# Kernel optimization log

Measured on AMD Instinct MI355X. Metric: run time of the kernel, lower is better.

Reference implementation:

```python
import jax, jax.numpy as jnp
import numpy as np

DIM = 256
QK = 256
HEADS = 8
NWIN = 16
TOPK = 4
MLP_RATIO = 4
SCALE = QK ** -0.5


def setup_inputs() -> dict:
    key = jax.random.key(0)
    ks = jax.random.split(key, 8)
    p = lambda k, shp: jax.random.normal(k, shp, jnp.float32) * 0.02
    hid = MLP_RATIO * DIM
    return {
        "x": jax.random.normal(ks[0], (8, DIM, 64, 64), jnp.float32),
        # to_q / to_kv : 1x1 Conv2d_BN (eval-mode BN with running stats 0/1 -> scale+shift)
        "wq": p(ks[1], (QK, DIM)), "gq": jnp.ones((QK,), jnp.float32), "bq": jnp.zeros((QK,), jnp.float32),
        "wkv": p(ks[2], (QK + DIM, DIM)), "gkv": jnp.ones((QK + DIM,), jnp.float32), "bkv": jnp.zeros((QK + DIM,), jnp.float32),
        # LEPE depthwise 5x5 conv
        "w_lepe": p(ks[3], (DIM, 1, 5, 5)), "b_lepe": jnp.zeros((DIM,), jnp.float32),
        # Mlp: fc1(1x1 Conv2d_BN) -> dwconv3x3 -> ReLU -> fc2(1x1 Conv2d_BN)
        "w_fc1": p(ks[4], (hid, DIM)), "g_fc1": jnp.ones((hid,), jnp.float32), "b_fc1": jnp.zeros((hid,), jnp.float32),
        "w_dw": p(ks[5], (hid, 1, 3, 3)), "b_dw": jnp.zeros((hid,), jnp.float32),
        "w_fc2": p(ks[6], (DIM, hid)), "g_fc2": jnp.ones((DIM,), jnp.float32), "b_fc2": jnp.zeros((DIM,), jnp.float32),
    }


def _dwconv(x, w, b, pad):
    # x: NCHW, w: (C,1,k,k) depthwise
    out = jax.lax.conv_general_dilated(
        x, w, (1, 1), [(pad, pad), (pad, pad)],
        feature_group_count=x.shape[1],
        dimension_numbers=("NCHW", "OIHW", "NCHW"))
    return out + b[None, :, None, None]


def _bra(x, wq, gq, bq, wkv, gkv, bkv, w_lepe, b_lepe):
    # Bi-Level Routing Attention. x: NCHW
    N, C, H, W = x.shape
    j = i = NWIN
    h, w_ = H // j, W // i          # per-window spatial (4,4)
    p2, w2 = j * i, h * w_          # 256 windows, 16 tokens/window
    xh = x.transpose(0, 2, 3, 1)    # NHWC
    # windowize: (N, p2, h, w, C)
    xw = xh.reshape(N, j, h, i, w_, C).transpose(0, 1, 3, 2, 4, 5).reshape(N, p2, h, w_, C)
    # 1x1 conv + BN(eval: stats 0/1) == matmul * gamma + beta
    q = (xw @ wq.T) * gq + bq                    # (N,p2,h,w,QK)
    kv = (xw @ wkv.T) * gkv + bkv                # (N,p2,h,w,QK+C)
    q_pix = q.reshape(N, p2, w2, QK)
    kv_pix = kv.reshape(N, p2, w2, QK + C)       # identity kv_down
    q_win = q.mean((2, 3))                       # (N,p2,QK)
    k_win = kv[..., :QK].mean((2, 3))            # (N,p2,QK)
    # LEPE on V in full-image layout
    v_img = kv[..., QK:].reshape(N, j, i, h, w_, C).transpose(0, 1, 3, 2, 4, 5).reshape(N, H, W, C)
    lepe = _dwconv(v_img.transpose(0, 3, 1, 2), w_lepe, b_lepe, 2).transpose(0, 2, 3, 1)  # NHWC
    # window-level topk routing (detached, non-differentiable)
    qd = jax.lax.stop_gradient(q_win)
    kd = jax.lax.stop_gradient(k_win)
    logit = (qd * SCALE) @ kd.transpose(0, 2, 1)            # (N,p2,p2)
    _, r_idx = jax.lax.top_k(logit, TOPK)                   # (N,p2,TOPK); r_weight unused (mul_weight='none')
    # gather selected KV windows: (N,p2,TOPK,w2,QK+C)
    kv_sel = jax.vmap(lambda kvp, idx: kvp[idx])(kv_pix, r_idx)
    ch_k, ch_v = QK // HEADS, C // HEADS
    k_sel = kv_sel[..., :QK].reshape(N, p2, TOPK * w2, HEADS, ch_k).transpose(0, 1, 3, 2, 4)
    v_sel = kv_sel[..., QK:].reshape(N, p2, TOPK * w2, HEADS, ch_v).transpose(0, 1, 3, 2, 4)
    qh = q_pix.reshape(N, p2, w2, HEADS, ch_k).transpose(0, 1, 3, 2, 4)
    attn = jax.nn.softmax(jnp.einsum("npmqc,npmkc->npmqk", qh * SCALE, k_sel), axis=-1)
    out = jnp.einsum("npmqk,npmkc->npmqc", attn, v_sel)     # (N,p2,HEADS,w2,ch_v)
    out = out.transpose(0, 1, 3, 2, 4).reshape(N, j, i, h, w_, C)
    out = out.transpose(0, 1, 3, 2, 4, 5).reshape(N, H, W, C)
    out = out + lepe                                         # wo = Identity
    return out.transpose(0, 3, 1, 2)                         # NCHW


def reference(x, wq, gq, bq, wkv, gkv, bkv, w_lepe, b_lepe,
              w_fc1, g_fc1, b_fc1, w_dw, b_dw, w_fc2, g_fc2, b_fc2):
    # top_Block: x = x + attn(x); x = x + mlp(x)   (drop_path inactive in eval)
    x = x + _bra(x, wq, gq, bq, wkv, gkv, bkv, w_lepe, b_lepe)
    h1 = jnp.einsum("nchw,dc->ndhw", x, w_fc1) * g_fc1[None, :, None, None] + b_fc1[None, :, None, None]
    h1 = jax.nn.relu(_dwconv(h1, w_dw, b_dw, 1))
    h2 = jnp.einsum("nchw,dc->ndhw", h1, w_fc2) * g_fc2[None, :, None, None] + b_fc2[None, :, None, None]
    return x + h2
```

## Files before the change

kernel.cpp:

```cpp
#include <hip/hip_runtime.h>
#include <hip/hip_bf16.h>

#define NBATCH 8
#define CDIM 256
#define HH 64
#define WW 64
#define HWSZ 4096
#define TT 32768
#define QKVD 768
#define TOPK 4
#define HID 1024
#define ATTN_SCALE 0.0625f

typedef __hip_bfloat16 bf16;
typedef __attribute__((ext_vector_type(8))) short s8v;
typedef __attribute__((ext_vector_type(4))) float f4v;

__device__ __forceinline__ float toF(bf16 v) { return __bfloat162float(v); }
__device__ __forceinline__ bf16  toB(float v) { return __float2bfloat16(v); }

__global__ void k_prep(const float* __restrict__ wq, const float* __restrict__ gq,
                       const float* __restrict__ wkv, const float* __restrict__ gkv,
                       const float* __restrict__ wfc1, const float* __restrict__ gfc1,
                       const float* __restrict__ wfc2, const float* __restrict__ gfc2,
                       const float* __restrict__ bq, const float* __restrict__ bkv,
                       const float* __restrict__ w_dw, const float* __restrict__ b_dw,
                       bf16* __restrict__ wbqkv, bf16* __restrict__ wbfc1,
                       bf16* __restrict__ wbfc2, float* __restrict__ bias768,
                       float* __restrict__ wdwT) {
    int i = blockIdx.x * 256 + threadIdx.x;
    if (i < 196608) {
        int r = i >> 8;
        float g = (r < 256) ? gq[r] : gkv[r - 256];
        float w = (r < 256) ? wq[i] : wkv[i - 65536];
        wbqkv[i] = toB(w * g);
        if (i < 768) bias768[i] = (i < 256) ? bq[i] : bkv[i - 256];
    } else if (i < 458752) {
        int j = i - 196608;
        wbfc1[j] = toB(wfc1[j] * gfc1[j >> 8]);
    } else if (i < 720896) {
        int j = i - 458752;
        wbfc2[j] = toB(wfc2[j] * gfc2[j >> 10]);
    } else if (i < 731136) {
        int j = i - 720896;
        int cg = j / 80, r = j - cg * 80;
        wdwT[j] = (r < 72) ? w_dw[(cg * 8 + r / 9) * 9 + (r % 9)]
                           : b_dw[cg * 8 + (r - 72)];
    }
}

__global__ void k_xt(const float* __restrict__ x, bf16* __restrict__ xt) {
    __shared__ float tile[32][33];
    int s0 = blockIdx.x * 32, c0 = blockIdx.y * 32, n = blockIdx.z;
    int tx = threadIdx.x, ty = threadIdx.y;
#pragma unroll
    for (int r = 0; r < 4; r++)
        tile[ty + r * 8][tx] = x[(size_t)n * CDIM * HWSZ + (size_t)(c0 + ty + r * 8) * HWSZ + s0 + tx];
    __syncthreads();
#pragma unroll
    for (int r = 0; r < 4; r++)
        xt[((size_t)n * HWSZ + s0 + ty + r * 8) * CDIM + c0 + tx] = toB(tile[tx][ty + r * 8]);
}

__global__ void k_xwin(const float* __restrict__ x, float* __restrict__ xwin) {
    int b = blockIdx.x;
    int n = b >> 8, c = b & 255;
    int p = threadIdx.x, wy = p >> 4, wx = p & 15;
    const float* pl = x + ((size_t)n * CDIM + c) * HWSZ;
    float s = 0.f;
#pragma unroll
    for (int dy = 0; dy < 4; dy++)
#pragma unroll
        for (int dx = 0; dx < 4; dx++)
            s += pl[(wy * 4 + dy) * WW + wx * 4 + dx];
    xwin[((size_t)(n << 8) + p) * 256 + c] = s * 0.0625f;
}

__global__ void k_qkwin(const float* __restrict__ xwin,
                        const float* __restrict__ wq, const float* __restrict__ wkv,
                        const float* __restrict__ gq, const float* __restrict__ bq,
                        const float* __restrict__ gkv, const float* __restrict__ bkv,
                        float* __restrict__ qkwin) {
    __shared__ float As[16][68];
    __shared__ float Bs[16][68];
    int m0 = blockIdx.x * 64, n0 = blockIdx.y * 64;
    int tid = threadIdx.x;
    int tx = tid & 15, ty = tid >> 4;
    float acc[4][4] = {};
    for (int k0 = 0; k0 < 256; k0 += 16) {
#pragma unroll
        for (int r = 0; r < 4; r++) {
            int lin = tid + r * 256;
            int row = lin >> 4, kk = lin & 15;
            As[kk][row] = xwin[(size_t)(m0 + row) * 256 + k0 + kk];
            int n = n0 + row;
            const float* wr = (n < 256) ? (wq + (size_t)n * 256) : (wkv + (size_t)(n - 256) * 256);
            Bs[kk][row] = wr[k0 + kk];
        }
        __syncthreads();
#pragma unroll
        for (int kk = 0; kk < 16; kk++) {
            float a[4], bb[4];
#pragma unroll
            for (int i = 0; i < 4; i++) a[i] = As[kk][tx * 4 + i];
#pragma unroll
            for (int j = 0; j < 4; j++) bb[j] = Bs[kk][ty * 4 + j];
#pragma unroll
            for (int i = 0; i < 4; i++)
#pragma unroll
                for (int j = 0; j < 4; j++) acc[i][j] += a[i] * bb[j];
        }
        __syncthreads();
    }
#pragma unroll
    for (int j = 0; j < 4; j++) {
        int n = n0 + ty * 4 + j;
        float gg = (n < 256) ? gq[n] : gkv[n - 256];
        float bb = (n < 256) ? bq[n] : bkv[n - 256];
#pragma unroll
        for (int i = 0; i < 4; i++)
            qkwin[(size_t)(m0 + tx * 4 + i) * 512 + n] = acc[i][j] * gg + bb;
    }
}

__global__ void k_logits(const float* __restrict__ qkwin, float* __restrict__ logits) {
    __shared__ float As[16][68];
    __shared__ float Bs[16][68];
    int m0 = blockIdx.x * 64, n0 = blockIdx.y * 64, img = blockIdx.z;
    const float* base = qkwin + (size_t)(img << 8) * 512;
    int tid = threadIdx.x;
    int tx = tid & 15, ty = tid >> 4;
    float acc[4][4] = {};
    for (int k0 = 0; k0 < 256; k0 += 16) {
#pragma unroll
        for (int r = 0; r < 4; r++) {
            int lin = tid + r * 256;
            int row = lin >> 4, kk = lin & 15;
            As[kk][row] = base[(size_t)(m0 + row) * 512 + k0 + kk];
            Bs[kk][row] = base[(size_t)(n0 + row) * 512 + 256 + k0 + kk];
        }
        __syncthreads();
#pragma unroll
        for (int kk = 0; kk < 16; kk++) {
            float a[4], bb[4];
#pragma unroll
            for (int i = 0; i < 4; i++) a[i] = As[kk][tx * 4 + i];
#pragma unroll
            for (int j = 0; j < 4; j++) bb[j] = Bs[kk][ty * 4 + j];
#pragma unroll
            for (int i = 0; i < 4; i++)
#pragma unroll
                for (int j = 0; j < 4; j++) acc[i][j] += a[i] * bb[j];
        }
        __syncthreads();
    }
    float* Lr = logits + (size_t)(img << 8) * 256;
#pragma unroll
    for (int j = 0; j < 4; j++)
#pragma unroll
        for (int i = 0; i < 4; i++)
            Lr[(size_t)(m0 + tx * 4 + i) * 256 + n0 + ty * 4 + j] = acc[i][j];
}

__global__ __launch_bounds__(256) void k_topk(const float* __restrict__ logits,
                                              int* __restrict__ topk) {
    int row = blockIdx.x * 4 + (threadIdx.x >> 6);
    int lane = threadIdx.x & 63;
    float4 v4 = *(const float4*)(logits + (size_t)row * 256 + lane * 4);
    float v[4] = {v4.x, v4.y, v4.z, v4.w};
#pragma unroll
    for (int sel = 0; sel < TOPK; sel++) {
        float mv = v[0]; int mi = lane * 4;
#pragma unroll
        for (int j = 1; j < 4; j++)
            if (v[j] > mv) { mv = v[j]; mi = lane * 4 + j; }
#pragma unroll
        for (int off = 1; off < 64; off <<= 1) {
            float ov = __shfl_xor(mv, off);
            int oi = __shfl_xor(mi, off);
            if (ov > mv || (ov == mv && oi < mi)) { mv = ov; mi = oi; }
        }
        if (lane == 0) topk[(size_t)row * TOPK + sel] = mi;
        if ((mi >> 2) == lane) v[mi & 3] = -INFINITY;
    }
}

template <int BM, int BN, int OUTMODE>
__global__ __launch_bounds__(256) void k_mfma(const bf16* __restrict__ A,
                                              const bf16* __restrict__ Wb,
                                              const float* __restrict__ bias,
                                              bf16* __restrict__ out,
                                              bf16* __restrict__ out2,
                                              int M, int N, int K) {
    constexpr int WROWS = BM / 2, WCOLS = BN / 2;
    constexpr int WM = WROWS / 16, WN = WCOLS / 16;
    constexpr int CA = (BM * 4) / 256;
    constexpr int CB = (BN * 4) / 256;
    __shared__ bf16 As[BM * 32];
    __shared__ bf16 Bs[BN * 32];
    int gx = gridDim.x;
    int lin = blockIdx.x + blockIdx.y * gx;
    int tot = gx * gridDim.y;
    int cpx = tot >> 3;
    int swz = (lin & 7) * cpx + (lin >> 3);
    int m0 = (swz % gx) * BM, n0 = (swz / gx) * BN;
    int tid = threadIdx.x;
    int w = tid >> 6, lane = tid & 63;
    int wr = w >> 1, wc = w & 1;
    int lm = lane & 15, lq = lane >> 4;
    f4v acc[WM][WN];
#pragma unroll
    for (int i = 0; i < WM; i++)
#pragma unroll
        for (int j = 0; j < WN; j++) acc[i][j] = (f4v){0.f, 0.f, 0.f, 0.f};

    for (int k0 = 0; k0 < K; k0 += 32) {
        s8v va[CA], vb[CB];
#pragma unroll
        for (int q = 0; q < CA; q++) {
            int c = tid + q * 256, row = c >> 2, col = c & 3;
            va[q] = *(const s8v*)(A + (size_t)(m0 + row) * K + k0 + col * 8);
        }
#pragma unroll
        for (int q = 0; q < CB; q++) {
            int c = tid + q * 256, row = c >> 2, col = c & 3;
            vb[q] = *(const s8v*)(Wb + (size_t)(n0 + row) * K + k0 + col * 8);
        }
        __syncthreads();
#pragma unroll
        for (int q = 0; q < CA; q++) {
            int c = tid + q * 256, row = c >> 2, col = c & 3;
            *(s8v*)&As[row * 32 + col * 8] = va[q];
        }
#pragma unroll
        for (int q = 0; q < CB; q++) {
            int c = tid + q * 256, row = c >> 2, col = c & 3;
            *(s8v*)&Bs[row * 32 + col * 8] = vb[q];
        }
        __syncthreads();
        s8v af[WM], bfr[WN];
#pragma unroll
        for (int i = 0; i < WM; i++)
            af[i] = *(const s8v*)&As[(wr * WROWS + i * 16 + lm) * 32 + lq * 8];
#pragma unroll
        for (int j = 0; j < WN; j++)
            bfr[j] = *(const s8v*)&Bs[(wc * WCOLS + j * 16 + lm) * 32 + lq * 8];
#pragma unroll
        for (int i = 0; i < WM; i++)
#pragma unroll
            for (int j = 0; j < WN; j++)
                acc[i][j] = __builtin_amdgcn_mfma_f32_16x16x32_bf16(af[i], bfr[j], acc[i][j], 0, 0, 0);
    }
#pragma unroll
    for (int j = 0; j < WN; j++) {
        int n = n0 + wc * WCOLS + j * 16 + lm;
        float bb = bias[n];
#pragma unroll
        for (int i = 0; i < WM; i++) {
            int mb = m0 + wr * WROWS + i * 16 + lq * 4;
#pragma unroll
            for (int r = 0; r < 4; r++)
                out[(size_t)(mb + r) * N + n] = toB(acc[i][j][r] + bb);
            if (OUTMODE == 1 && n >= 512) {
                bf16* dst = out2 + ((size_t)(mb >> 12) * CDIM + (n - 512)) * HWSZ + (mb & 4095);
#pragma unroll
                for (int r = 0; r < 4; r++) dst[r] = toB(acc[i][j][r] + bb);
            }
        }
    }
}

__global__ void k_lepe_pl(bf16* __restrict__ vpl, const float* __restrict__ w_lepe,
                          const float* __restrict__ b_lepe) {
    __shared__ float pl[HWSZ];
    int b = blockIdx.x;
    int n = b >> 8, c = b & 255;
    int tid = threadIdx.x;
    bf16* plane = vpl + ((size_t)n * CDIM + c) * HWSZ;
    const uint4* p4 = (const uint4*)plane;
#pragma unroll
    for (int k = 0; k < 2; k++) {
        uint4 v = p4[tid + k * 256];
        const bf16* pv = (const bf16*)&v;
        int base = (tid + k * 256) * 8;
#pragma unroll
        for (int e = 0; e < 8; e++) pl[base + e] = toF(pv[e]);
    }
    float wreg[25];
#pragma unroll
    for (int i = 0; i < 25; i++) wreg[i] = w_lepe[c * 25 + i];
    float bias = b_lepe[c];
    __syncthreads();
#pragma unroll
    for (int k = 0; k < 2; k++) {
        int s = (tid + k * 256) * 8;
        int y = s >> 6, x0 = s & 63;
        uint4 pk;
        bf16* pb = (bf16*)&pk;
#pragma unroll
        for (int e = 0; e < 8; e++) {
            int xb = x0 + e;
            float acc = bias;
#pragma unroll
            for (int dy = -2; dy <= 2; dy++) {
                int yy = y + dy;
                if (yy < 0 || yy >= HH) continue;
#pragma unroll
                for (int dx = -2; dx <= 2; dx++) {
                    int xx = xb + dx;
                    if (xx < 0 || xx >= WW) continue;
                    acc += pl[yy * 64 + xx] * wreg[(dy + 2) * 5 + (dx + 2)];
                }
            }
            pb[e] = toB(acc);
        }
        ((uint4*)plane)[tid + k * 256] = pk;
    }
}

__global__ __launch_bounds__(256) void k_attn(const bf16* __restrict__ qkv,
                                              const int* __restrict__ topk,
                                              bf16* __restrict__ attnout) {
    __shared__ bf16 vst[256][72];
    __shared__ bf16 plds[4][16][72];
    __shared__ float lsm[4][16];
    __shared__ int toks[64];
    int b = blockIdx.x;
    int n = b >> 8, p = b & 255;
    int wy = p >> 4, wx = p & 15;
    int tid = threadIdx.x;
    if (tid < 64) {
        int rp = topk[((size_t)(n << 8) + p) * TOPK + (tid >> 4)] & 255;
        int st = tid & 15;
        toks[tid] = ((rp >> 4) * 4 + (st >> 2)) * WW + (rp & 15) * 4 + (st & 3);
    }
    __syncthreads();
    const bf16* qbase = qkv + (size_t)n * HWSZ * QKVD;
    {
        int kt = tid & 63, jj = tid >> 6;
#pragma unroll
        for (int pass = 0; pass < 8; pass++) {
            int d0 = pass * 32 + jj * 8;
            uint4 v = *(const uint4*)(qbase + (size_t)toks[kt] * QKVD + 512 + d0);
            const bf16* pv = (const bf16*)&v;
#pragma unroll
            for (int e = 0; e < 8; e++) vst[d0 + e][kt] = pv[e];
        }
    }
    __syncthreads();
    int w = tid >> 6, lane = tid & 63;
    int ln = lane & 15, lq = lane >> 4;
    int myS = (wy * 4 + (ln >> 2)) * WW + wx * 4 + (ln & 3);
    const f4v fz = {0.f, 0.f, 0.f, 0.f};
    for (int hh = 0; hh < 2; hh++) {
        int h = w * 2 + hh;
        s8v qf = *(const s8v*)(qbase + (size_t)myS * QKVD + h * 32 + lq * 8);
        f4v st4[4];
#pragma unroll
        for (int t = 0; t < 4; t++) {
            s8v kf = *(const s8v*)(qbase + (size_t)toks[t * 16 + ln] * QKVD + 256 + h * 32 + lq * 8);
            st4[t] = __builtin_amdgcn_mfma_f32_16x16x32_bf16(kf, qf, fz, 0, 0, 0);
        }
        float mx = -INFINITY;
#pragma unroll
        for (int t = 0; t < 4; t++)
#pragma unroll
            for (int r = 0; r < 4; r++) mx = fmaxf(mx, st4[t][r]);
        mx = fmaxf(mx, __shfl_xor(mx, 16));
        mx = fmaxf(mx, __shfl_xor(mx, 32));
        mx *= ATTN_SCALE;
        float sum = 0.f;
#pragma unroll
        for (int t = 0; t < 4; t++)
#pragma unroll
            for (int r = 0; r < 4; r++) {
                float pp = __expf(st4[t][r] * ATTN_SCALE - mx);
                sum += pp;
                plds[w][ln][t * 16 + lq * 4 + r] = toB(pp);
            }
        sum += __shfl_xor(sum, 16);
        sum += __shfl_xor(sum, 32);
        if (lq == 0) lsm[w][ln] = sum;
        __syncthreads();
        s8v ap0 = *(const s8v*)&plds[w][ln][lq * 8];
        s8v ap1 = *(const s8v*)&plds[w][ln][32 + lq * 8];
#pragma unroll
        for (int dt = 0; dt < 2; dt++) {
            int dim = h * 32 + dt * 16 + ln;
            s8v vv0 = *(const s8v*)&vst[dim][lq * 8];
            s8v vv1 = *(const s8v*)&vst[dim][32 + lq * 8];
            f4v o = __builtin_amdgcn_mfma_f32_16x16x32_bf16(ap0, vv0, fz, 0, 0, 0);
            o = __builtin_amdgcn_mfma_f32_16x16x32_bf16(ap1, vv1, o, 0, 0, 0);
#pragma unroll
            for (int r = 0; r < 4; r++) {
                int t = lq * 4 + r;
                float linv = 1.f / lsm[w][t];
                int s = (wy * 4 + (t >> 2)) * WW + wx * 4 + (t & 3);
                attnout[((size_t)n * HWSZ + s) * CDIM + dim] = toB(o[r] * linv);
            }
        }
        __syncthreads();
    }
}

__global__ void k_x1(const bf16* __restrict__ xt, const bf16* __restrict__ lepe,
                     const bf16* __restrict__ attnout, bf16* __restrict__ x1) {
    __shared__ float tile[32][33];
    int s0 = blockIdx.x * 32, c0 = blockIdx.y * 32, n = blockIdx.z;
    int tx = threadIdx.x, ty = threadIdx.y;
#pragma unroll
    for (int r = 0; r < 4; r++) {
        int c = c0 + ty + r * 8;
        tile[ty + r * 8][tx] = toF(lepe[((size_t)n * CDIM + c) * HWSZ + s0 + tx]);
    }
    __syncthreads();
#pragma unroll
    for (int r = 0; r < 4; r++) {
        int s = s0 + ty + r * 8;
        size_t idx = ((size_t)n * HWSZ + s) * CDIM + c0 + tx;
        x1[idx] = toB(toF(xt[idx]) + toF(attnout[idx]) + tile[tx][ty + r * 8]);
    }
}

__global__ __launch_bounds__(256) void k_dw3_t(const bf16* __restrict__ h1,
                                               const float* __restrict__ wdwT,
                                               bf16* __restrict__ h1p) {
    int tid = threadIdx.x;
    int cg = tid & 127;
    int slot = tid >> 7;
    int seg = blockIdx.x;
    int img = blockIdx.y;
    int y = seg >> 2;
    int x0 = ((seg & 3) << 4) + (slot << 3);
    const float* wp = wdwT + cg * 80;
    float w[72], bias[8];
#pragma unroll
    for (int i = 0; i < 72; i++) w[i] = wp[i];
#pragma unroll
    for (int c = 0; c < 8; c++) bias[c] = wp[72 + c];
    const uint4* src = (const uint4*)h1 + (size_t)img * HWSZ * 128;
    uint4* dst = (uint4*)h1p + (size_t)img * HWSZ * 128;
#pragma unroll
    for (int xi = 0; xi < 8; xi++) {
        int x = x0 + xi;
        float o[8];
#pragma unroll
        for (int c = 0; c < 8; c++) o[c] = bias[c];
#pragma unroll
        for (int dy = -1; dy <= 1; dy++) {
            int yy = y + dy;
            if (yy < 0 || yy >= HH) continue;
#pragma unroll
            for (int dx = -1; dx <= 1; dx++) {
                int xx = x + dx;
                if (xx < 0 || xx >= WW) continue;
                int k = (dy + 1) * 3 + (dx + 1);
                uint4 v = src[(size_t)(yy * WW + xx) * 128 + cg];
                const bf16* pv = (const bf16*)&v;
#pragma unroll
                for (int c = 0; c < 8; c++) o[c] += toF(pv[c]) * w[c * 9 + k];
            }
        }
        uint4 pk;
        bf16* pb = (bf16*)&pk;
#pragma unroll
        for (int c = 0; c < 8; c++) pb[c] = toB(fmaxf(o[c], 0.f));
        dst[(size_t)(y * WW + x) * 128 + cg] = pk;
    }
}

__global__ void k_final(const bf16* __restrict__ x1, const bf16* __restrict__ h2,
                        float* __restrict__ out) {
    __shared__ float tile[32][33];
    int s0 = blockIdx.x * 32, c0 = blockIdx.y * 32, n = blockIdx.z;
    int tx = threadIdx.x, ty = threadIdx.y;
#pragma unroll
    for (int r = 0; r < 4; r++) {
        int s = s0 + ty + r * 8;
        size_t idx = ((size_t)n * HWSZ + s) * CDIM + c0 + tx;
        tile[tx][ty + r * 8] = toF(x1[idx]) + toF(h2[idx]);
    }
    __syncthreads();
#pragma unroll
    for (int r = 0; r < 4; r++) {
        int c = c0 + ty + r * 8;
        out[(size_t)n * CDIM * HWSZ + (size_t)c * HWSZ + s0 + tx] = tile[ty + r * 8][tx];
    }
}

extern "C" void kernel_launch(void* const* d_in, const int* in_sizes, int n_in,
                              void* d_out, int out_size, void* d_ws, size_t ws_size,
                              hipStream_t stream) {
    (void)in_sizes; (void)n_in; (void)out_size; (void)ws_size;
    const float* x      = (const float*)d_in[0];
    const float* wq     = (const float*)d_in[1];
    const float* gq     = (const float*)d_in[2];
    const float* bq     = (const float*)d_in[3];
    const float* wkv    = (const float*)d_in[4];
    const float* gkv    = (const float*)d_in[5];
    const float* bkv    = (const float*)d_in[6];
    const float* w_lepe = (const float*)d_in[7];
    const float* b_lepe = (const float*)d_in[8];
    const float* w_fc1  = (const float*)d_in[9];
    const float* g_fc1  = (const float*)d_in[10];
    const float* b_fc1  = (const float*)d_in[11];
    const float* w_dw   = (const float*)d_in[12];
    const float* b_dw   = (const float*)d_in[13];
    const float* w_fc2  = (const float*)d_in[14];
    const float* g_fc2  = (const float*)d_in[15];
    const float* b_fc2  = (const float*)d_in[16];

    char* ws = (char*)d_ws;
    bf16*  qkv    = (bf16*)(ws);
    bf16*  vpl    = (bf16*)(ws + 50331648);
    bf16*  attn   = (bf16*)(ws + 67108864);
    bf16*  xt     = (bf16*)(ws + 83886080);
    bf16*  x1     = (bf16*)(ws + 83886080);
    bf16*  h1     = (bf16*)(ws);
    bf16*  h1p    = (bf16*)(ws + 33554432);
    bf16*  h2     = (bf16*)(ws + 67108864);
    float* xwin   = (float*)(ws + 100663296);
    float* qkwin  = (float*)(ws + 102760448);
    int*   tk     = (int*)(ws + 106954752);
    bf16*  wbqkv  = (bf16*)(ws + 106987520);
    bf16*  wbfc1  = (bf16*)(ws + 107380736);
    bf16*  wbfc2  = (bf16*)(ws + 107905024);
    float* bias768= (float*)(ws + 108429312);
    float* wdwT   = (float*)(ws + 108433408);
    float* logits = (float*)(ws + 108478464);

    k_prep<<<2856, 256, 0, stream>>>(wq, gq, wkv, gkv, w_fc1, g_fc1, w_fc2, g_fc2,
                                     bq, bkv, w_dw, b_dw,
                                     wbqkv, wbfc1, wbfc2, bias768, wdwT);
    k_xt<<<dim3(128, 8, 8), dim3(32, 8), 0, stream>>>(x, xt);
    k_xwin<<<2048, 256, 0, stream>>>(x, xwin);
    k_qkwin<<<dim3(32, 8), 256, 0, stream>>>(xwin, wq, wkv, gq, bq, gkv, bkv, qkwin);
    k_logits<<<dim3(4, 4, 8), 256, 0, stream>>>(qkwin, logits);
    k_topk<<<512, 256, 0, stream>>>(logits, tk);
    k_mfma<128, 128, 1><<<dim3(256, 6), 256, 0, stream>>>(
        xt, wbqkv, bias768, qkv, vpl, TT, QKVD, CDIM);
    k_lepe_pl<<<2048, 256, 0, stream>>>(vpl, w_lepe, b_lepe);
    k_attn<<<2048, 256, 0, stream>>>(qkv, tk, attn);
    k_x1<<<dim3(128, 8, 8), dim3(32, 8), 0, stream>>>(xt, vpl, attn, x1);
    for (int c = 0; c < 2; c++) {
        bf16* x1c = x1 + (size_t)c * 16384 * CDIM;
        bf16* h2c = h2 + (size_t)c * 16384 * CDIM;
        k_mfma<128, 128, 0><<<dim3(128, 8), 256, 0, stream>>>(
            x1c, wbfc1, b_fc1, h1, nullptr, 16384, HID, CDIM);
        k_dw3_t<<<dim3(256, 4), 256, 0, stream>>>(h1, wdwT, h1p);
        k_mfma<64, 128, 0><<<dim3(256, 2), 256, 0, stream>>>(
            h1p, wbfc2, b_fc2, h2c, nullptr, 16384, CDIM, HID);
    }
    k_final<<<dim3(128, 8, 8), dim3(32, 8), 0, stream>>>(x1, h2, (float*)d_out);
}
```

Measured before the change: 469.3 us.

## Use direct global-to-LDS loads in GEMM and compute LEPE channels-last

The GEMM kernel now loads A and B tiles straight into LDS with global_load_lds, so the data no longer passes through registers on its way to shared memory. A trailing barrier is added so each tile is fully consumed before the next one overwrites it. The planar V copy written by the QKV GEMM is gone: the LEPE 5x5 depthwise conv now reads V directly from the token-major qkv buffer and writes a channels-last output. That lets k_x1 become a plain vectorized elementwise add with no transpose. The trade-off is that the LEPE kernel reads its neighbourhood from global memory with strided 8-byte loads instead of from a shared-memory plane, and holds 100 weights in registers per thread.

Result: slower. 487.1 us (+3.8%).

```diff
diff --git a/kernel.cpp b/kernel.cpp
--- a/kernel.cpp
+++ b/kernel.cpp
@@ -18,6 +18,12 @@
 
 __device__ __forceinline__ float toF(bf16 v) { return __bfloat162float(v); }
 __device__ __forceinline__ bf16  toB(float v) { return __float2bfloat16(v); }
+
+__device__ __forceinline__ void gload_lds16(const bf16* g, bf16* l) {
+    __builtin_amdgcn_global_load_lds(
+        (const __attribute__((address_space(1))) void*)g,
+        (__attribute__((address_space(3))) void*)l, 16, 0, 0);
+}
 
 __global__ void k_prep(const float* __restrict__ wq, const float* __restrict__ gq,
                        const float* __restrict__ wkv, const float* __restrict__ gkv,
@@ -185,12 +191,11 @@
     }
 }
 
-template <int BM, int BN, int OUTMODE>
+template <int BM, int BN>
 __global__ __launch_bounds__(256) void k_mfma(const bf16* __restrict__ A,
                                               const bf16* __restrict__ Wb,
                                               const float* __restrict__ bias,
                                               bf16* __restrict__ out,
-                                              bf16* __restrict__ out2,
                                               int M, int N, int K) {
     constexpr int WROWS = BM / 2, WCOLS = BN / 2;
     constexpr int WM = WROWS / 16, WN = WCOLS / 16;
@@ -215,28 +220,19 @@
         for (int j = 0; j < WN; j++) acc[i][j] = (f4v){0.f, 0.f, 0.f, 0.f};
 
     for (int k0 = 0; k0 < K; k0 += 32) {
-        s8v va[CA], vb[CB];
 #pragma unroll
         for (int q = 0; q < CA; q++) {
             int c = tid + q * 256, row = c >> 2, col = c & 3;
-            va[q] = *(const s8v*)(A + (size_t)(m0 + row) * K + k0 + col * 8);
+            gload_lds16(A + (size_t)(m0 + row) * K + k0 + col * 8,
+                        As + (size_t)(w * 64 + q * 256) * 8);
         }
 #pragma unroll
         for (int q = 0; q < CB; q++) {
             int c = tid + q * 256, row = c >> 2, col = c & 3;
-            vb[q] = *(const s8v*)(Wb + (size_t)(n0 + row) * K + k0 + col * 8);
-        }
-        __syncthreads();
-#pragma unroll
-        for (int q = 0; q < CA; q++) {
-            int c = tid + q * 256, row = c >> 2, col = c & 3;
-            *(s8v*)&As[row * 32 + col * 8] = va[q];
-        }
-#pragma unroll
-        for (int q = 0; q < CB; q++) {
-            int c = tid + q * 256, row = c >> 2, col = c & 3;
-            *(s8v*)&Bs[row * 32 + col * 8] = vb[q];
-        }
+            gload_lds16(Wb + (size_t)(n0 + row) * K + k0 + col * 8,
+                        Bs + (size_t)(w * 64 + q * 256) * 8);
+        }
+        asm volatile("s_waitcnt vmcnt(0)" ::: "memory");
         __syncthreads();
         s8v af[WM], bfr[WN];
 #pragma unroll
@@ -250,6 +246,7 @@
 #pragma unroll
             for (int j = 0; j < WN; j++)
                 acc[i][j] = __builtin_amdgcn_mfma_f32_16x16x32_bf16(af[i], bfr[j], acc[i][j], 0, 0, 0);
+        __syncthreads();
     }
 #pragma unroll
     for (int j = 0; j < WN; j++) {
@@ -261,60 +258,52 @@
 #pragma unroll
             for (int r = 0; r < 4; r++)
                 out[(size_t)(mb + r) * N + n] = toB(acc[i][j][r] + bb);
-            if (OUTMODE == 1 && n >= 512) {
-                bf16* dst = out2 + ((size_t)(mb >> 12) * CDIM + (n - 512)) * HWSZ + (mb & 4095);
-#pragma unroll
-                for (int r = 0; r < 4; r++) dst[r] = toB(acc[i][j][r] + bb);
+        }
+    }
+}
+
+__global__ __launch_bounds__(256) void k_lepe_t(const bf16* __restrict__ qkv,
+                                                const float* __restrict__ w_lepe,
+                                                const float* __restrict__ b_lepe,
+                                                bf16* __restrict__ lepe) {
+    int tid = threadIdx.x;
+    int cg = tid & 63;
+    int slot = tid >> 6;
+    int bx = blockIdx.x;
+    int n = blockIdx.y;
+    int y = bx >> 1;
+    int x0 = (bx & 1) * 32 + slot * 8;
+    float w[100], bias[4];
+#pragma unroll
+    for (int i = 0; i < 100; i++) w[i] = w_lepe[cg * 100 + i];
+#pragma unroll
+    for (int c = 0; c < 4; c++) bias[c] = b_lepe[cg * 4 + c];
+    const bf16* vb = qkv + (size_t)n * HWSZ * QKVD + 512;
+    bf16* dst = lepe + (size_t)n * HWSZ * CDIM;
+#pragma unroll
+    for (int xi = 0; xi < 8; xi++) {
+        int x = x0 + xi;
+        float o[4] = {bias[0], bias[1], bias[2], bias[3]};
+#pragma unroll
+        for (int dy = -2; dy <= 2; dy++) {
+            int yy = y + dy;
+            if (yy < 0 || yy >= HH) continue;
+#pragma unroll
+            for (int dx = -2; dx <= 2; dx++) {
+                int xx = x + dx;
+                if (xx < 0 || xx >= WW) continue;
+                int k = (dy + 2) * 5 + (dx + 2);
+                uint2 v = *(const uint2*)(vb + (size_t)(yy * WW + xx) * QKVD + cg * 4);
+                const bf16* pv = (const bf16*)&v;
+#pragma unroll
+                for (int c = 0; c < 4; c++) o[c] += toF(pv[c]) * w[c * 25 + k];
             }
         }
-    }
-}
-
-__global__ void k_lepe_pl(bf16* __restrict__ vpl, const float* __restrict__ w_lepe,
-                          const float* __restrict__ b_lepe) {
-    __shared__ float pl[HWSZ];
-    int b = blockIdx.x;
-    int n = b >> 8, c = b & 255;
-    int tid = threadIdx.x;
-    bf16* plane = vpl + ((size_t)n * CDIM + c) * HWSZ;
-    const uint4* p4 = (const uint4*)plane;
-#pragma unroll
-    for (int k = 0; k < 2; k++) {
-        uint4 v = p4[tid + k * 256];
-        const bf16* pv = (const bf16*)&v;
-        int base = (tid + k * 256) * 8;
-#pragma unroll
-        for (int e = 0; e < 8; e++) pl[base + e] = toF(pv[e]);
-    }
-    float wreg[25];
-#pragma unroll
-    for (int i = 0; i < 25; i++) wreg[i] = w_lepe[c * 25 + i];
-    float bias = b_lepe[c];
-    __syncthreads();
-#pragma unroll
-    for (int k = 0; k < 2; k++) {
-        int s = (tid + k * 256) * 8;
-        int y = s >> 6, x0 = s & 63;
-        uint4 pk;
+        uint2 pk;
         bf16* pb = (bf16*)&pk;
 #pragma unroll
-        for (int e = 0; e < 8; e++) {
-            int xb = x0 + e;
-            float acc = bias;
-#pragma unroll
-            for (int dy = -2; dy <= 2; dy++) {
-                int yy = y + dy;
-                if (yy < 0 || yy >= HH) continue;
-#pragma unroll
-                for (int dx = -2; dx <= 2; dx++) {
-                    int xx = xb + dx;
-                    if (xx < 0 || xx >= WW) continue;
-                    acc += pl[yy * 64 + xx] * wreg[(dy + 2) * 5 + (dx + 2)];
-                }
-            }
-            pb[e] = toB(acc);
-        }
-        ((uint4*)plane)[tid + k * 256] = pk;
+        for (int c = 0; c < 4; c++) pb[c] = toB(o[c]);
+        *(uint2*)(dst + (size_t)(y * WW + x) * CDIM + cg * 4) = pk;
     }
 }
 
@@ -403,23 +392,22 @@
     }
 }
 
-__global__ void k_x1(const bf16* __restrict__ xt, const bf16* __restrict__ lepe,
-                     const bf16* __restrict__ attnout, bf16* __restrict__ x1) {
-    __shared__ float tile[32][33];
-    int s0 = blockIdx.x * 32, c0 = blockIdx.y * 32, n = blockIdx.z;
-    int tx = threadIdx.x, ty = threadIdx.y;
-#pragma unroll
-    for (int r = 0; r < 4; r++) {
-        int c = c0 + ty + r * 8;
-        tile[ty + r * 8][tx] = toF(lepe[((size_t)n * CDIM + c) * HWSZ + s0 + tx]);
-    }
-    __syncthreads();
-#pragma unroll
-    for (int r = 0; r < 4; r++) {
-        int s = s0 + ty + r * 8;
-        size_t idx = ((size_t)n * HWSZ + s) * CDIM + c0 + tx;
-        x1[idx] = toB(toF(xt[idx]) + toF(attnout[idx]) + tile[tx][ty + r * 8]);
-    }
+__global__ __launch_bounds__(256) void k_x1(const bf16* __restrict__ xt,
+                                            const bf16* __restrict__ lepe,
+                                            const bf16* __restrict__ attnout,
+                                            bf16* __restrict__ x1) {
+    size_t i = ((size_t)blockIdx.x * 256 + threadIdx.x) * 8;
+    uint4 a = *(const uint4*)(xt + i);
+    uint4 b = *(const uint4*)(attnout + i);
+    uint4 c = *(const uint4*)(lepe + i);
+    const bf16* pa = (const bf16*)&a;
+    const bf16* pb = (const bf16*)&b;
+    const bf16* pc = (const bf16*)&c;
+    uint4 r;
+    bf16* pr = (bf16*)&r;
+#pragma unroll
+    for (int e = 0; e < 8; e++) pr[e] = toB(toF(pa[e]) + toF(pb[e]) + toF(pc[e]));
+    *(uint4*)(x1 + i) = r;
 }
 
 __global__ __launch_bounds__(256) void k_dw3_t(const bf16* __restrict__ h1,
@@ -512,7 +500,7 @@
 
     char* ws = (char*)d_ws;
     bf16*  qkv    = (bf16*)(ws);
-    bf16*  vpl    = (bf16*)(ws + 50331648);
+    bf16*  lepe   = (bf16*)(ws + 50331648);
     bf16*  attn   = (bf16*)(ws + 67108864);
     bf16*  xt     = (bf16*)(ws + 83886080);
     bf16*  x1     = (bf16*)(ws + 83886080);
@@ -537,19 +525,19 @@
     k_qkwin<<<dim3(32, 8), 256, 0, stream>>>(xwin, wq, wkv, gq, bq, gkv, bkv, qkwin);
     k_logits<<<dim3(4, 4, 8), 256, 0, stream>>>(qkwin, logits);
     k_topk<<<512, 256, 0, stream>>>(logits, tk);
-    k_mfma<128, 128, 1><<<dim3(256, 6), 256, 0, stream>>>(
-        xt, wbqkv, bias768, qkv, vpl, TT, QKVD, CDIM);
-    k_lepe_pl<<<2048, 256, 0, stream>>>(vpl, w_lepe, b_lepe);
+    k_mfma<128, 128><<<dim3(256, 6), 256, 0, stream>>>(
+        xt, wbqkv, bias768, qkv, TT, QKVD, CDIM);
+    k_lepe_t<<<dim3(128, 8), 256, 0, stream>>>(qkv, w_lepe, b_lepe, lepe);
     k_attn<<<2048, 256, 0, stream>>>(qkv, tk, attn);
-    k_x1<<<dim3(128, 8, 8), dim3(32, 8), 0, stream>>>(xt, vpl, attn, x1);
+    k_x1<<<4096, 256, 0, stream>>>(xt, lepe, attn, x1);
     for (int c = 0; c < 2; c++) {
         bf16* x1c = x1 + (size_t)c * 16384 * CDIM;
         bf16* h2c = h2 + (size_t)c * 16384 * CDIM;
-        k_mfma<128, 128, 0><<<dim3(128, 8), 256, 0, stream>>>(
-            x1c, wbfc1, b_fc1, h1, nullptr, 16384, HID, CDIM);
+        k_mfma<128, 128><<<dim3(128, 8), 256, 0, stream>>>(
+            x1c, wbfc1, b_fc1, h1, 16384, HID, CDIM);
         k_dw3_t<<<dim3(256, 4), 256, 0, stream>>>(h1, wdwT, h1p);
-        k_mfma<64, 128, 0><<<dim3(256, 2), 256, 0, stream>>>(
-            h1p, wbfc2, b_fc2, h2c, nullptr, 16384, CDIM, HID);
+        k_mfma<64, 128><<<dim3(256, 2), 256, 0, stream>>>(
+            h1p, wbfc2, b_fc2, h2c, 16384, CDIM, HID);
     }
     k_final<<<dim3(128, 8, 8), dim3(32, 8), 0, stream>>>(x1, h2, (float*)d_out);
 }
```
